# Performance work log

Hardware: AMD Instinct MI355X
Metric: run time of the kernel (lower is better)

The kernel has to match this reference:

```python
import jax, jax.numpy as jnp
import numpy as np

N, E = 20000, 100000
D_IN, H1, C1 = 512, 8, 64   # conv1: 512 -> 8 heads x 64, concat -> 512
H2, C2 = 4, 128             # conv2: 512 -> 4 heads x 128, mean -> 128


def setup_inputs() -> dict:
    key = jax.random.key(0)
    k = jax.random.split(key, 12)
    s_in = 1.0 / np.sqrt(D_IN).astype(np.float32)
    return {
        "street_embedding": jax.random.normal(k[0], (N, D_IN), jnp.float32),
        "edge_index": jax.random.randint(k[1], (2, E), 0, N),
        "y": jax.random.randint(k[2], (N,), 0, C2),
        "train_mask": jax.random.bernoulli(k[3], 0.5, (N,)),
        "W1": jax.random.normal(k[4], (D_IN, H1 * C1), jnp.float32) * s_in,
        "att_src1": jax.random.normal(k[5], (H1, C1), jnp.float32) * 0.1,
        "att_dst1": jax.random.normal(k[6], (H1, C1), jnp.float32) * 0.1,
        "b1": jnp.zeros((H1 * C1,), jnp.float32),
        "W2": jax.random.normal(k[7], (H1 * C1, H2 * C2), jnp.float32) * s_in,
        "att_src2": jax.random.normal(k[8], (H2, C2), jnp.float32) * 0.1,
        "att_dst2": jax.random.normal(k[9], (H2, C2), jnp.float32) * 0.1,
        "b2": jnp.zeros((C2,), jnp.float32),
    }


def _gat_conv(x, W, a_src, a_dst, b, src, dst, n, H, C, concat):
    # linear transform (no bias, as in PyG GATConv's internal lin)
    xp = (x @ W).reshape(n, H, C)                      # [N,H,C]
    asrc = jnp.einsum('nhc,hc->nh', xp, a_src)         # [N,H]
    adst = jnp.einsum('nhc,hc->nh', xp, a_dst)
    e = jax.nn.leaky_relu(asrc[src] + adst[dst], 0.2)  # [E',H] edge scores
    # softmax over incoming edges per destination node
    m = jax.lax.stop_gradient(jax.ops.segment_max(e, dst, num_segments=n))
    ex = jnp.exp(e - m[dst])
    denom = jax.ops.segment_sum(ex, dst, num_segments=n)
    alpha = ex / (denom[dst] + 1e-16)                  # [E',H]
    out = jax.ops.segment_sum(alpha[:, :, None] * xp[src], dst, num_segments=n)  # [N,H,C]
    if concat:
        return out.reshape(n, H * C) + b
    return out.mean(axis=1) + b


def reference(street_embedding, edge_index, y, train_mask,
              W1, att_src1, att_dst1, b1, W2, att_src2, att_dst2, b2):
    n = street_embedding.shape[0]
    loop = jnp.arange(n)
    # PyG GATConv adds self-loops by default
    src = jnp.concatenate([edge_index[0], loop])
    dst = jnp.concatenate([edge_index[1], loop])
    # dropout layers are identity in eval mode
    h = _gat_conv(street_embedding, W1, att_src1, att_dst1, b1, src, dst, n, H1, C1, True)
    h = jax.nn.elu(h)
    out = _gat_conv(h, W2, att_src2, att_dst2, b2, src, dst, n, H2, C2, False)  # [N,C2]
    # CrossEntropyLoss, mean over train_mask nodes (weighted mean, jit-safe)
    logp = jax.nn.log_softmax(out, axis=-1)
    ce = -jnp.take_along_axis(logp, y[:, None], axis=-1)[:, 0]
    w = train_mask.astype(out.dtype)
    loss_su = jnp.sum(w * ce) / jnp.sum(w)
    return (loss_su, out)
```

## Files before the change

kernel.cpp:

```cpp
#include <hip/hip_runtime.h>
#include <cmath>

#define D_IN 512
#define HC   512
#define NH1  8
#define NC1  64
#define NH2  4
#define NC2  128
#define BM 128
#define BN 128
#define BK 64

typedef __attribute__((ext_vector_type(8))) short short8;
typedef __attribute__((ext_vector_type(8))) unsigned short u16x8;
typedef __attribute__((ext_vector_type(8))) unsigned short ushort8;
typedef __attribute__((ext_vector_type(4))) float f32x4;

__device__ inline ushort f2bf(float f) {
  unsigned u = __float_as_uint(f);
  return (ushort)((u + 0x7FFFu + ((u >> 16) & 1u)) >> 16);
}
__device__ inline float bf2f(ushort b) { return __uint_as_float(((unsigned)b) << 16); }

__global__ void k_pre(const float* __restrict__ x, ushort* __restrict__ Abf,
                      const float* __restrict__ W1, const float* __restrict__ W2,
                      ushort* __restrict__ Wt1, ushort* __restrict__ Wt2, int n4x,
                      const int* __restrict__ ei, int E, int Etot,
                      int* __restrict__ cnt) {
  __shared__ float tl[64][65];
  int t = threadIdx.x;
  int bx = blockIdx.x;
  int nxb = (n4x + 255) >> 8;
  if (bx < nxb) {
    int i = bx * 256 + t;
    if (i < n4x) {
      float4 v = ((const float4*)x)[i];
      ushort4 r = { f2bf(v.x), f2bf(v.y), f2bf(v.z), f2bf(v.w) };
      ((ushort4*)Abf)[i] = r;
    }
  } else if (bx < nxb + 128) {
    int b = bx - nxb;
    int w = b >> 6, tile = b & 63;
    int k0 = (tile >> 3) * 64, n0 = (tile & 7) * 64;
    const float* W = w ? W2 : W1;
    ushort* Wt = w ? Wt2 : Wt1;
    int r = t >> 2, q = t & 3;
    const float4* src = (const float4*)(W + (size_t)(k0 + r) * HC + n0 + q * 16);
#pragma unroll
    for (int j = 0; j < 4; ++j) {
      float4 v = src[j];
      tl[r][q * 16 + 4 * j + 0] = v.x;
      tl[r][q * 16 + 4 * j + 1] = v.y;
      tl[r][q * 16 + 4 * j + 2] = v.z;
      tl[r][q * 16 + 4 * j + 3] = v.w;
    }
    __syncthreads();
    ushort8* dst = (ushort8*)(Wt + (size_t)(n0 + r) * D_IN + k0 + q * 16);
#pragma unroll
    for (int j = 0; j < 2; ++j) {
      ushort8 o;
#pragma unroll
      for (int c = 0; c < 8; ++c) o[c] = f2bf(tl[q * 16 + 8 * j + c][r]);
      dst[j] = o;
    }
  } else {
    int e = (bx - nxb - 128) * 256 + t;
    if (e >= Etot) return;
    int d = (e < E) ? ei[E + e] : e - E;
    atomicAdd(&cnt[d], 1);
  }
}

template<int H, int SCAN>
__global__ void k_gemm_bf16(const ushort* __restrict__ A, const ushort* __restrict__ Bt,
                            ushort* __restrict__ Cbf,
                            const float* __restrict__ att_s, const float* __restrict__ att_d,
                            float* __restrict__ asrc, float* __restrict__ adst, int M,
                            const int* __restrict__ cnt, int* __restrict__ rowstart, int Nn) {
  constexpr int C = HC / H;
  __shared__ __align__(16) ushort As[BM * BK];
  __shared__ __align__(16) ushort Bs[BN * BK];
  int t = threadIdx.x;

  if (SCAN && blockIdx.x == 0) {
    int* sA = (int*)As;
    int* sB = (int*)Bs;
    int lane = t & 63, w = t >> 6;
    const int4* c4 = (const int4*)cnt;
    int nb4 = (Nn + 3) >> 2;
    int T4 = (nb4 + 255) >> 8;
    if (T4 <= 20) {
      for (int i = 0; i < T4; ++i) {
        int g = i * 256 + t;
        int s = 0;
        if (g < nb4) { int4 v = c4[g]; s = v.x + v.y + v.z + v.w; }
        (g < 4096 ? sA[g] : sB[g - 4096]) = s;
      }
      __syncthreads();
      int base = t * T4;
      int S = 0;
      for (int i = 0; i < T4; ++i) {
        int g = base + i;
        if (g < nb4) S += (g < 4096 ? sA[g] : sB[g - 4096]);
      }
      int v = S;
#pragma unroll
      for (int off = 1; off < 64; off <<= 1) {
        int u = __shfl_up(v, off);
        if (lane >= off) v += u;
      }
      if (lane == 63) sB[3000 + w] = v;
      __syncthreads();
      int wp = 0;
#pragma unroll
      for (int i = 0; i < 4; ++i) if (i < w) wp += sB[3000 + i];
      int run = wp + v - S;
      for (int i = 0; i < T4; ++i) {
        int g = base + i;
        if (g < nb4) {
          int c = (g < 4096 ? sA[g] : sB[g - 4096]);
          (g < 4096 ? sA[g] : sB[g - 4096]) = run;
          run += c;
        }
      }
      __syncthreads();
      for (int i = 0; i < T4; ++i) {
        int g = i * 256 + t;
        if (g < nb4) {
          int4 v = c4[g];
          int p = (g < 4096 ? sA[g] : sB[g - 4096]);
          int jb = g * 4;
          if (jb + 0 < Nn) rowstart[jb + 0] = p;  p += v.x;
          if (jb + 1 < Nn) rowstart[jb + 1] = p;  p += v.y;
          if (jb + 2 < Nn) rowstart[jb + 2] = p;  p += v.z;
          if (jb + 3 < Nn) rowstart[jb + 3] = p;  p += v.w;
          if (jb + 4 >= Nn) rowstart[Nn] = p;
        }
      }
    } else {
      int T = (Nn + 255) / 256;
      int base = t * T;
      int sum = 0;
      for (int i = 0; i < T; ++i) { int j = base + i; if (j < Nn) sum += cnt[j]; }
      int v = sum;
#pragma unroll
      for (int off = 1; off < 64; off <<= 1) {
        int u = __shfl_up(v, off);
        if (lane >= off) v += u;
      }
      if (lane == 63) sB[3000 + w] = v;
      __syncthreads();
      int wp = 0;
#pragma unroll
      for (int i = 0; i < 4; ++i) if (i < w) wp += sB[3000 + i];
      int run = wp + v - sum;
      for (int i = 0; i < T; ++i) {
        int j = base + i;
        if (j < Nn) { rowstart[j] = run; run += cnt[j]; }
      }
      if (t == 255) rowstart[Nn] = run;
    }
    return;
  }

  int lin = blockIdx.x - (SCAN ? 1 : 0);
  int nwg = gridDim.x - (SCAN ? 1 : 0);
  int q = nwg >> 3, r = nwg & 7;
  int xcd = lin & 7, pos = lin >> 3;
  int wg = (xcd < r ? xcd * (q + 1) : r * (q + 1) + (xcd - r) * q) + pos;
  int m0 = (wg >> 2) * BM;
  int n0 = (wg & 3) * BN;

  int wave = t >> 6, lane = t & 63;
  int ln = lane & 15, qd = lane >> 4;
  int wm = (wave >> 1) * 64, wn = (wave & 1) * 64;

  f32x4 acc[4][4] = {};

  int g = t >> 6, ct = (t >> 4) & 3, lt = t & 15;
  int rA0 = m0 + g * 16 + lt;      if (rA0 > M - 1) rA0 = M - 1;
  int rA1 = m0 + 64 + g * 16 + lt; if (rA1 > M - 1) rA1 = M - 1;
  const ushort* gA0 = A + (size_t)rA0 * D_IN + ct * 8;
  const ushort* gA1 = A + (size_t)rA1 * D_IN + ct * 8;
  const ushort* gB0 = Bt + (size_t)(n0 + g * 16 + lt) * D_IN + ct * 8;
  const ushort* gB1 = Bt + (size_t)(n0 + 64 + g * 16 + lt) * D_IN + ct * 8;

  for (int k0 = 0; k0 < D_IN; k0 += BK) {
    __syncthreads();
#pragma unroll
    for (int h = 0; h < 2; ++h) {
      int ko = k0 + h * 32;
      int lo = h * 4096;
      __builtin_amdgcn_global_load_lds(
          (const __attribute__((address_space(1))) void*)(gA0 + ko),
          (__attribute__((address_space(3))) void*)(As + lo + t * 8), 16, 0, 0);
      __builtin_amdgcn_global_load_lds(
          (const __attribute__((address_space(1))) void*)(gA1 + ko),
          (__attribute__((address_space(3))) void*)(As + lo + 2048 + t * 8), 16, 0, 0);
      __builtin_amdgcn_global_load_lds(
          (const __attribute__((address_space(1))) void*)(gB0 + ko),
          (__attribute__((address_space(3))) void*)(Bs + lo + t * 8), 16, 0, 0);
      __builtin_amdgcn_global_load_lds(
          (const __attribute__((address_space(1))) void*)(gB1 + ko),
          (__attribute__((address_space(3))) void*)(Bs + lo + 2048 + t * 8), 16, 0, 0);
    }
    __syncthreads();
#pragma unroll
    for (int h = 0; h < 2; ++h) {
      int lo = h * 4096;
      short8 a[4], bb[4];
#pragma unroll
      for (int i = 0; i < 4; ++i)
        a[i] = *(const short8*)&As[lo + (((wave >> 1) * 4 + i) * 4 + qd) * 128 + ln * 8];
#pragma unroll
      for (int j = 0; j < 4; ++j)
        bb[j] = *(const short8*)&Bs[lo + (((wave & 1) * 4 + j) * 4 + qd) * 128 + ln * 8];
#pragma unroll
      for (int i = 0; i < 4; ++i)
#pragma unroll
        for (int j = 0; j < 4; ++j)
          acc[i][j] = __builtin_amdgcn_mfma_f32_16x16x32_bf16(a[i], bb[j], acc[i][j], 0, 0, 0);
    }
  }

#pragma unroll
  for (int i = 0; i < 4; ++i) {
#pragma unroll
    for (int reg = 0; reg < 4; ++reg) {
      int row = m0 + wm + i * 16 + qd * 4 + reg;
      if (row >= M) continue;
#pragma unroll
      for (int j = 0; j < 4; ++j)
        Cbf[(size_t)row * HC + n0 + wn + j * 16 + ln] = f2bf(acc[i][j][reg]);
    }
  }

  int colbase = n0 + wn;
  int h = colbase / C;
  float sa[4], da[4];
#pragma unroll
  for (int j = 0; j < 4; ++j) {
    int c = (colbase % C) + j * 16 + ln;
    sa[j] = att_s[h * C + c];
    da[j] = att_d[h * C + c];
  }
#pragma unroll
  for (int i = 0; i < 4; ++i) {
#pragma unroll
    for (int reg = 0; reg < 4; ++reg) {
      float ps = acc[i][0][reg] * sa[0] + acc[i][1][reg] * sa[1]
               + acc[i][2][reg] * sa[2] + acc[i][3][reg] * sa[3];
      float pd = acc[i][0][reg] * da[0] + acc[i][1][reg] * da[1]
               + acc[i][2][reg] * da[2] + acc[i][3][reg] * da[3];
#pragma unroll
      for (int o = 1; o < 16; o <<= 1) { ps += __shfl_xor(ps, o); pd += __shfl_xor(pd, o); }
      int row = m0 + wm + i * 16 + qd * 4 + reg;
      if (ln == 0 && row < M) {
        if (C == 64) {
          asrc[(size_t)h * M + row] = ps;
          adst[(size_t)h * M + row] = pd;
        } else {
          int sub = (colbase >> 6) & 1;
          asrc[(row * H + h) * 2 + sub] = ps;
          adst[(row * H + h) * 2 + sub] = pd;
        }
      }
    }
  }
}

__global__ void k_scatter(const int* __restrict__ ei, int E, int Etot,
                          const int* __restrict__ rowstart, int* __restrict__ cursor,
                          int* __restrict__ csr_src) {
  int e = blockIdx.x * blockDim.x + threadIdx.x;
  if (e >= Etot) return;
  int s = (e < E) ? ei[e] : e - E;
  int d = (e < E) ? ei[E + e] : e - E;
  int pos = atomicAdd(&cursor[d], 1);
  csr_src[rowstart[d] + pos] = s;
}

__global__ void k_agg1(const int* __restrict__ rowstart, const int* __restrict__ csr_src,
                       const float* __restrict__ asrc, const float* __restrict__ adst,
                       const ushort* __restrict__ xp, ushort* __restrict__ hout,
                       const float* __restrict__ bias, int N) {
  int wv = threadIdx.x >> 6, lane = threadIdx.x & 63;
  int s = blockIdx.x & 7;
  int n = (blockIdx.x >> 3) * 4 + wv;
  if (n >= N) return;
  int grp = lane >> 3, li = lane & 7;
  int beg = rowstart[n], end = rowstart[n + 1];
  float adn = adst[(size_t)s * N + n];
  const float* as_s = asrc + (size_t)s * N;
  const ushort* xs = xp + s * NC1 + li * 8;

  float acc[8] = {};
  float wsum = 0.f;
  for (int c0 = beg; c0 < end; c0 += 64) {
    int len = end - c0; if (len > 64) len = 64;
    int ev = (lane < len) ? csr_src[c0 + lane] : 0;
    for (int j = 0; j < len; j += 8) {
      int idx = j + grp;
      bool val = idx < len;
      int src = __shfl(ev, val ? idx : 0);
      float v = as_s[src] + adn;
      v = (v > 0.f) ? v : 0.2f * v;
      float w = val ? __expf(v) : 0.f;
      u16x8 a = *(const u16x8*)(xs + (size_t)src * HC);
#pragma unroll
      for (int k = 0; k < 8; ++k) acc[k] += w * bf2f(a[k]);
      wsum += w;
    }
  }
#pragma unroll
  for (int o = 8; o < 64; o <<= 1) {
    wsum += __shfl_xor(wsum, o);
#pragma unroll
    for (int k = 0; k < 8; ++k) acc[k] += __shfl_xor(acc[k], o);
  }
  if (grp == 0) {
    float rdn = 1.0f / (wsum + 1e-16f);
    u16x8 rr;
#pragma unroll
    for (int k = 0; k < 8; ++k) {
      float v = acc[k] * rdn + bias[s * NC1 + li * 8 + k];
      v = (v > 0.f) ? v : expm1f(v);
      rr[k] = f2bf(v);
    }
    __builtin_nontemporal_store(rr, (u16x8*)(hout + (size_t)n * HC + s * NC1 + li * 8));
  }
}

__global__ void k_agg2(const int* __restrict__ rowstart, const int* __restrict__ csr_src,
                       const float* __restrict__ asrc, const float* __restrict__ adst,
                       const ushort* __restrict__ xp,
                       float* __restrict__ out2, const float* __restrict__ bias,
                       const int* __restrict__ y, const int* __restrict__ msk,
                       float* __restrict__ acc2, int N) {
  constexpr int H = NH2;
  int wv = threadIdx.x >> 6, lane = threadIdx.x & 63;
  int n = blockIdx.x * 4 + wv;
  if (n >= N) return;
  int h = lane >> 4;
  int beg = rowstart[n], end = rowstart[n + 1];

  float2 t2 = ((const float2*)adst)[n * H + h];
  float adn = t2.x + t2.y;

  float acc[8] = {};
  float wsum = 0.f;

#define SCR(s_)  (((const float2*)asrc)[(s_) * H + h].x + \
                  ((const float2*)asrc)[(s_) * H + h].y)
#define EDGE(w_, a_)  do {                                   \
    float ww = (w_);                                         \
    _Pragma("unroll") for (int k = 0; k < 8; ++k)            \
      acc[k] += ww * bf2f((a_)[k]);                          \
    wsum += ww; } while (0)
#define LRELU(v_) ((v_) > 0.f ? (v_) : 0.2f * (v_))

  for (int c0 = beg; c0 < end; c0 += 64) {
    int len = end - c0; if (len > 64) len = 64;
    int ev = (lane < len) ? csr_src[c0 + lane] : 0;
    int j = 0;
    for (; j + 3 < len; j += 4) {
      int s0 = __shfl(ev, j), s1 = __shfl(ev, j + 1);
      int s2 = __shfl(ev, j + 2), s3 = __shfl(ev, j + 3);
      float v0 = SCR(s0) + adn, v1 = SCR(s1) + adn;
      float v2 = SCR(s2) + adn, v3 = SCR(s3) + adn;
      u16x8 a0 = ((const u16x8*)xp)[(size_t)s0 * 64 + lane];
      u16x8 a1 = ((const u16x8*)xp)[(size_t)s1 * 64 + lane];
      u16x8 a2 = ((const u16x8*)xp)[(size_t)s2 * 64 + lane];
      u16x8 a3 = ((const u16x8*)xp)[(size_t)s3 * 64 + lane];
      EDGE(__expf(LRELU(v0)), a0);
      EDGE(__expf(LRELU(v1)), a1);
      EDGE(__expf(LRELU(v2)), a2);
      EDGE(__expf(LRELU(v3)), a3);
    }
    for (; j + 1 < len; j += 2) {
      int s0 = __shfl(ev, j), s1 = __shfl(ev, j + 1);
      float v0 = SCR(s0) + adn, v1 = SCR(s1) + adn;
      u16x8 a0 = ((const u16x8*)xp)[(size_t)s0 * 64 + lane];
      u16x8 a1 = ((const u16x8*)xp)[(size_t)s1 * 64 + lane];
      EDGE(__expf(LRELU(v0)), a0);
      EDGE(__expf(LRELU(v1)), a1);
    }
    if (j < len) {
      int s0 = __shfl(ev, j);
      float v0 = SCR(s0) + adn;
      u16x8 a0 = ((const u16x8*)xp)[(size_t)s0 * 64 + lane];
      EDGE(__expf(LRELU(v0)), a0);
    }
  }
#undef SCR
#undef EDGE
#undef LRELU

  float rdn = 1.0f / (wsum + 1e-16f);
#pragma unroll
  for (int k = 0; k < 8; ++k) acc[k] *= rdn;

#pragma unroll
  for (int k = 0; k < 8; ++k) {
    float v = acc[k];
    v += __shfl_xor(v, 16);
    v += __shfl_xor(v, 32);
    acc[k] = v * 0.25f + bias[(lane & 15) * 8 + k];
  }
  if (lane < 16) {
    int cb = lane * 8;
#pragma unroll
    for (int k = 0; k < 8; ++k) out2[(size_t)n * NC2 + cb + k] = acc[k];
  }
  float mx = acc[0];
#pragma unroll
  for (int k = 1; k < 8; ++k) mx = fmaxf(mx, acc[k]);
#pragma unroll
  for (int o = 1; o < 16; o <<= 1) mx = fmaxf(mx, __shfl_xor(mx, o));
  float e = 0.f;
#pragma unroll
  for (int k = 0; k < 8; ++k) e += __expf(acc[k] - mx);
#pragma unroll
  for (int o = 1; o < 16; o <<= 1) e += __shfl_xor(e, o);
  int yv = y[n];
  float sel = acc[0];
#pragma unroll
  for (int k = 1; k < 8; ++k) sel = ((yv & 7) == k) ? acc[k] : sel;
  float vy = __shfl(sel, yv >> 3);
  if (lane == 0 && msk[n] != 0) {
    float ce = mx + logf(e) - vy;
    int slot = n & 127;
    atomicAdd(&acc2[slot], ce);
    atomicAdd(&acc2[128 + slot], 1.0f);
  }
}

__global__ void k_final(const float* __restrict__ acc2, float* __restrict__ out0) {
  int tid = threadIdx.x;
  float ce = acc2[tid], ct = acc2[128 + tid];
#pragma unroll
  for (int o = 32; o > 0; o >>= 1) { ce += __shfl_xor(ce, o); ct += __shfl_xor(ct, o); }
  __shared__ float s[4];
  if ((tid & 63) == 0) { s[(tid >> 6) * 2] = ce; s[(tid >> 6) * 2 + 1] = ct; }
  __syncthreads();
  if (tid == 0) out0[0] = (s[0] + s[2]) / (s[1] + s[3]);
}

extern "C" void kernel_launch(void* const* d_in, const int* in_sizes, int n_in,
                              void* d_out, int out_size, void* d_ws, size_t ws_size,
                              hipStream_t stream) {
  const float* x   = (const float*)d_in[0];
  const int*   ei  = (const int*)d_in[1];
  const int*   y   = (const int*)d_in[2];
  const int*   msk = (const int*)d_in[3];
  const float* W1  = (const float*)d_in[4];
  const float* as1 = (const float*)d_in[5];
  const float* ad1 = (const float*)d_in[6];
  const float* b1  = (const float*)d_in[7];
  const float* W2  = (const float*)d_in[8];
  const float* as2 = (const float*)d_in[9];
  const float* ad2 = (const float*)d_in[10];
  const float* b2  = (const float*)d_in[11];
  float* out = (float*)d_out;

  int N = in_sizes[0] / D_IN;
  int E = in_sizes[1] / 2;
  int Etot = E + N;

  float* ws = (float*)d_ws;
  size_t NF = (size_t)N * HC;
  float* asr1 = ws;
  float* adt1 = asr1 + (size_t)N * NH1;
  float* asr2 = adt1 + (size_t)N * NH1;
  float* adt2 = asr2 + (size_t)N * 2 * NH2;
  float* acc2 = adt2 + (size_t)N * 2 * NH2;
  int*   cnt    = (int*)(acc2 + 256);
  int*   cursor = cnt + N;
  size_t zero_bytes = (256 + 2 * (size_t)N) * sizeof(float);
  int*   rowstart = cursor + N;
  int*   csr_src  = rowstart + N + 1;
  ushort* xpbf = (ushort*)((((uintptr_t)(csr_src + Etot)) + 15) & ~(uintptr_t)15);
  ushort* Abf = xpbf + NF;
  ushort* Wt1 = Abf + NF;
  ushort* Wt2 = Wt1 + (size_t)D_IN * HC;

  hipMemsetAsync(acc2, 0, zero_bytes, stream);

  int n4x = (int)(NF / 4);
  int nxb = (n4x + 255) / 256;
  int nhb = (Etot + 255) / 256;
  k_pre<<<nxb + 128 + nhb, 256, 0, stream>>>(x, Abf, W1, W2, Wt1, Wt2, n4x,
                                             ei, E, Etot, cnt);

  int nwg = (HC / BN) * ((N + BM - 1) / BM);
  int agg1blocks = 8 * ((N + 3) / 4);
  int agg2blocks = (N + 3) / 4;

  k_gemm_bf16<NH1, 1><<<nwg + 1, 256, 0, stream>>>(Abf, Wt1, xpbf, as1, ad1, asr1, adt1, N,
                                                   cnt, rowstart, N);
  k_scatter<<<(Etot + 255) / 256, 256, 0, stream>>>(ei, E, Etot, rowstart, cursor, csr_src);
  k_agg1<<<agg1blocks, 256, 0, stream>>>(rowstart, csr_src, asr1, adt1, xpbf, Abf, b1, N);

  k_gemm_bf16<NH2, 0><<<nwg, 256, 0, stream>>>(Abf, Wt2, xpbf, as2, ad2, asr2, adt2, N,
                                               nullptr, nullptr, N);
  k_agg2<<<agg2blocks, 256, 0, stream>>>(rowstart, csr_src, asr2, adt2, xpbf,
                                         out + 1, b2, y, msk, acc2, N);

  k_final<<<1, 128, 0, stream>>>(acc2, out);
}
```

Baseline: 331.5 us.

## Restructure layer-1 aggregation to wave-per-node with node-major scores; fuse final loss

Layer-1 attention scores are now stored node-major ([N,H]) instead of head-major. k_agg1 changes from one wave per (node, head) slice to one wave per node, where each lane handles 8 channels across all heads, and it reuses the unrolled 4-edge loop from k_agg2. This cuts redundant CSR index loads and gives wide coalesced row gathers. The separate k_final launch is removed: the last wave to finish in k_agg2, detected through an atomic arrival counter, reduces the loss partials. That saves one launch but adds a global atomic per wave and relies on threadfence ordering.

```diff
diff --git a/kernel.cpp b/kernel.cpp
--- a/kernel.cpp
+++ b/kernel.cpp
@@ -257,8 +257,7 @@
       int row = m0 + wm + i * 16 + qd * 4 + reg;
       if (ln == 0 && row < M) {
         if (C == 64) {
-          asrc[(size_t)h * M + row] = ps;
-          adst[(size_t)h * M + row] = pd;
+          asrc[row * H + h] = ps; adst[row * H + h] = pd;
         } else {
           int sub = (colbase >> 6) & 1;
           asrc[(row * H + h) * 2 + sub] = ps;
@@ -285,73 +284,17 @@
                        const ushort* __restrict__ xp, ushort* __restrict__ hout,
                        const float* __restrict__ bias, int N) {
   int wv = threadIdx.x >> 6, lane = threadIdx.x & 63;
-  int s = blockIdx.x & 7;
-  int n = (blockIdx.x >> 3) * 4 + wv;
+  int n = blockIdx.x * 4 + wv;
   if (n >= N) return;
-  int grp = lane >> 3, li = lane & 7;
+  int h = lane >> 3;
   int beg = rowstart[n], end = rowstart[n + 1];
-  float adn = adst[(size_t)s * N + n];
-  const float* as_s = asrc + (size_t)s * N;
-  const ushort* xs = xp + s * NC1 + li * 8;
+
+  float adn = adst[n * NH1 + h];
 
   float acc[8] = {};
   float wsum = 0.f;
-  for (int c0 = beg; c0 < end; c0 += 64) {
-    int len = end - c0; if (len > 64) len = 64;
-    int ev = (lane < len) ? csr_src[c0 + lane] : 0;
-    for (int j = 0; j < len; j += 8) {
-      int idx = j + grp;
-      bool val = idx < len;
-      int src = __shfl(ev, val ? idx : 0);
-      float v = as_s[src] + adn;
-      v = (v > 0.f) ? v : 0.2f * v;
-      float w = val ? __expf(v) : 0.f;
-      u16x8 a = *(const u16x8*)(xs + (size_t)src * HC);
-#pragma unroll
-      for (int k = 0; k < 8; ++k) acc[k] += w * bf2f(a[k]);
-      wsum += w;
-    }
-  }
-#pragma unroll
-  for (int o = 8; o < 64; o <<= 1) {
-    wsum += __shfl_xor(wsum, o);
-#pragma unroll
-    for (int k = 0; k < 8; ++k) acc[k] += __shfl_xor(acc[k], o);
-  }
-  if (grp == 0) {
-    float rdn = 1.0f / (wsum + 1e-16f);
-    u16x8 rr;
-#pragma unroll
-    for (int k = 0; k < 8; ++k) {
-      float v = acc[k] * rdn + bias[s * NC1 + li * 8 + k];
-      v = (v > 0.f) ? v : expm1f(v);
-      rr[k] = f2bf(v);
-    }
-    __builtin_nontemporal_store(rr, (u16x8*)(hout + (size_t)n * HC + s * NC1 + li * 8));
-  }
-}
-
-__global__ void k_agg2(const int* __restrict__ rowstart, const int* __restrict__ csr_src,
-                       const float* __restrict__ asrc, const float* __restrict__ adst,
-                       const ushort* __restrict__ xp,
-                       float* __restrict__ out2, const float* __restrict__ bias,
-                       const int* __restrict__ y, const int* __restrict__ msk,
-                       float* __restrict__ acc2, int N) {
-  constexpr int H = NH2;
-  int wv = threadIdx.x >> 6, lane = threadIdx.x & 63;
-  int n = blockIdx.x * 4 + wv;
-  if (n >= N) return;
-  int h = lane >> 4;
-  int beg = rowstart[n], end = rowstart[n + 1];
-
-  float2 t2 = ((const float2*)adst)[n * H + h];
-  float adn = t2.x + t2.y;
-
-  float acc[8] = {};
-  float wsum = 0.f;
-
-#define SCR(s_)  (((const float2*)asrc)[(s_) * H + h].x + \
-                  ((const float2*)asrc)[(s_) * H + h].y)
+
+#define SCR(s_)  (asrc[(s_) * NH1 + h])
 #define EDGE(w_, a_)  do {                                   \
     float ww = (w_);                                         \
     _Pragma("unroll") for (int k = 0; k < 8; ++k)            \
@@ -393,6 +336,87 @@
     }
   }
 #undef SCR
+
+  float rdn = 1.0f / (wsum + 1e-16f);
+#pragma unroll
+  for (int k = 0; k < 8; ++k) acc[k] *= rdn;
+
+  int c = lane * 8;
+  u16x8 rr;
+#pragma unroll
+  for (int k = 0; k < 8; ++k) {
+    float v = acc[k] + bias[c + k];
+    v = (v > 0.f) ? v : expm1f(v);
+    rr[k] = f2bf(v);
+  }
+  ((u16x8*)hout)[(size_t)n * 64 + lane] = rr;
+#undef EDGE
+#undef LRELU
+}
+
+__global__ void k_agg2(const int* __restrict__ rowstart, const int* __restrict__ csr_src,
+                       const float* __restrict__ asrc, const float* __restrict__ adst,
+                       const ushort* __restrict__ xp,
+                       float* __restrict__ out2, const float* __restrict__ bias,
+                       const int* __restrict__ y, const int* __restrict__ msk,
+                       float* __restrict__ acc2, int N,
+                       float* __restrict__ out0, int* __restrict__ syncv) {
+  constexpr int H = NH2;
+  int wv = threadIdx.x >> 6, lane = threadIdx.x & 63;
+  int n = blockIdx.x * 4 + wv;
+  if (n >= N) return;
+  int h = lane >> 4;
+  int beg = rowstart[n], end = rowstart[n + 1];
+
+  float2 t2 = ((const float2*)adst)[n * H + h];
+  float adn = t2.x + t2.y;
+
+  float acc[8] = {};
+  float wsum = 0.f;
+
+#define SCR(s_)  (((const float2*)asrc)[(s_) * H + h].x + \
+                  ((const float2*)asrc)[(s_) * H + h].y)
+#define EDGE(w_, a_)  do {                                   \
+    float ww = (w_);                                         \
+    _Pragma("unroll") for (int k = 0; k < 8; ++k)            \
+      acc[k] += ww * bf2f((a_)[k]);                          \
+    wsum += ww; } while (0)
+#define LRELU(v_) ((v_) > 0.f ? (v_) : 0.2f * (v_))
+
+  for (int c0 = beg; c0 < end; c0 += 64) {
+    int len = end - c0; if (len > 64) len = 64;
+    int ev = (lane < len) ? csr_src[c0 + lane] : 0;
+    int j = 0;
+    for (; j + 3 < len; j += 4) {
+      int s0 = __shfl(ev, j), s1 = __shfl(ev, j + 1);
+      int s2 = __shfl(ev, j + 2), s3 = __shfl(ev, j + 3);
+      float v0 = SCR(s0) + adn, v1 = SCR(s1) + adn;
+      float v2 = SCR(s2) + adn, v3 = SCR(s3) + adn;
+      u16x8 a0 = ((const u16x8*)xp)[(size_t)s0 * 64 + lane];
+      u16x8 a1 = ((const u16x8*)xp)[(size_t)s1 * 64 + lane];
+      u16x8 a2 = ((const u16x8*)xp)[(size_t)s2 * 64 + lane];
+      u16x8 a3 = ((const u16x8*)xp)[(size_t)s3 * 64 + lane];
+      EDGE(__expf(LRELU(v0)), a0);
+      EDGE(__expf(LRELU(v1)), a1);
+      EDGE(__expf(LRELU(v2)), a2);
+      EDGE(__expf(LRELU(v3)), a3);
+    }
+    for (; j + 1 < len; j += 2) {
+      int s0 = __shfl(ev, j), s1 = __shfl(ev, j + 1);
+      float v0 = SCR(s0) + adn, v1 = SCR(s1) + adn;
+      u16x8 a0 = ((const u16x8*)xp)[(size_t)s0 * 64 + lane];
+      u16x8 a1 = ((const u16x8*)xp)[(size_t)s1 * 64 + lane];
+      EDGE(__expf(LRELU(v0)), a0);
+      EDGE(__expf(LRELU(v1)), a1);
+    }
+    if (j < len) {
+      int s0 = __shfl(ev, j);
+      float v0 = SCR(s0) + adn;
+      u16x8 a0 = ((const u16x8*)xp)[(size_t)s0 * 64 + lane];
+      EDGE(__expf(LRELU(v0)), a0);
+    }
+  }
+#undef SCR
 #undef EDGE
 #undef LRELU
 
@@ -433,17 +457,18 @@
     atomicAdd(&acc2[slot], ce);
     atomicAdd(&acc2[128 + slot], 1.0f);
   }
-}
-
-__global__ void k_final(const float* __restrict__ acc2, float* __restrict__ out0) {
-  int tid = threadIdx.x;
-  float ce = acc2[tid], ct = acc2[128 + tid];
-#pragma unroll
-  for (int o = 32; o > 0; o >>= 1) { ce += __shfl_xor(ce, o); ct += __shfl_xor(ct, o); }
-  __shared__ float s[4];
-  if ((tid & 63) == 0) { s[(tid >> 6) * 2] = ce; s[(tid >> 6) * 2 + 1] = ct; }
-  __syncthreads();
-  if (tid == 0) out0[0] = (s[0] + s[2]) / (s[1] + s[3]);
+
+  __threadfence();
+  int arrived = 0;
+  if (lane == 0) arrived = atomicAdd(&syncv[0], 1) + 1;
+  arrived = __shfl(arrived, 0);
+  if (arrived == N) {
+    float ce = atomicAdd(&acc2[lane], 0.0f) + atomicAdd(&acc2[64 + lane], 0.0f);
+    float ct = atomicAdd(&acc2[128 + lane], 0.0f) + atomicAdd(&acc2[192 + lane], 0.0f);
+#pragma unroll
+    for (int o = 32; o > 0; o >>= 1) { ce += __shfl_xor(ce, o); ct += __shfl_xor(ct, o); }
+    if (lane == 0) out0[0] = ce / ct;
+  }
 }
 
 extern "C" void kernel_launch(void* const* d_in, const int* in_sizes, int n_in,
@@ -474,9 +499,10 @@
   float* asr2 = adt1 + (size_t)N * NH1;
   float* adt2 = asr2 + (size_t)N * 2 * NH2;
   float* acc2 = adt2 + (size_t)N * 2 * NH2;
-  int*   cnt    = (int*)(acc2 + 256);
+  int*   syncv  = (int*)(acc2 + 256);
+  int*   cnt    = syncv + 16;
   int*   cursor = cnt + N;
-  size_t zero_bytes = (256 + 2 * (size_t)N) * sizeof(float);
+  size_t zero_bytes = (256 + 16 + 2 * (size_t)N) * sizeof(float);
   int*   rowstart = cursor + N;
   int*   csr_src  = rowstart + N + 1;
   ushort* xpbf = (ushort*)((((uintptr_t)(csr_src + Etot)) + 15) & ~(uintptr_t)15);
@@ -493,18 +519,16 @@
                                              ei, E, Etot, cnt);
 
   int nwg = (HC / BN) * ((N + BM - 1) / BM);
-  int agg1blocks = 8 * ((N + 3) / 4);
-  int agg2blocks = (N + 3) / 4;
+  int aggblocks = (N + 3) / 4;
 
   k_gemm_bf16<NH1, 1><<<nwg + 1, 256, 0, stream>>>(Abf, Wt1, xpbf, as1, ad1, asr1, adt1, N,
                                                    cnt, rowstart, N);
   k_scatter<<<(Etot + 255) / 256, 256, 0, stream>>>(ei, E, Etot, rowstart, cursor, csr_src);
-  k_agg1<<<agg1blocks, 256, 0, stream>>>(rowstart, csr_src, asr1, adt1, xpbf, Abf, b1, N);
+  k_agg1<<<aggblocks, 256, 0, stream>>>(rowstart, csr_src, asr1, adt1, xpbf, Abf, b1, N);
 
   k_gemm_bf16<NH2, 0><<<nwg, 256, 0, stream>>>(Abf, Wt2, xpbf, as2, ad2, asr2, adt2, N,
                                                nullptr, nullptr, N);
-  k_agg2<<<agg2blocks, 256, 0, stream>>>(rowstart, csr_src, asr2, adt2, xpbf,
-                                         out + 1, b2, y, msk, acc2, N);
-
-  k_final<<<1, 128, 0, stream>>>(acc2, out);
-}
+  k_agg2<<<aggblocks, 256, 0, stream>>>(rowstart, csr_src, asr2, adt2, xpbf,
+                                        out + 1, b2, y, msk, acc2, N,
+                                        out, syncv);
+}
```

Measured after the change: 1.067 ms. 222% more time.
